# Performance work log

Measured on AMD Instinct MI355X. Metric: run time of the kernel, lower is better.

## Reference

```python
import jax, jax.numpy as jnp
import numpy as np

EPS_NORM = 1e-6
EPS_LN = 1e-5


def setup_inputs() -> dict:
    key = jax.random.key(0)
    ks = jax.random.split(key, 6)
    b, m, d = 8, 1024, 768
    n, p = 64, 16
    h = 2 * d
    x = jax.random.normal(ks[0], (b, m, d), dtype=jnp.float32)
    phi = jax.random.normal(ks[1], (n, p, d), dtype=jnp.float32)
    # per-expert LayerNorm affine params
    ln_g = jnp.ones((n, d), dtype=jnp.float32)
    ln_b = jnp.zeros((n, d), dtype=jnp.float32)
    # per-expert MLP weights (torch Linear default init ~ U(-1/sqrt(fan_in), ...); use scaled normal)
    w1 = jax.random.normal(ks[2], (n, d, h), dtype=jnp.float32) * (1.0 / np.sqrt(d))
    b1 = jax.random.normal(ks[3], (n, h), dtype=jnp.float32) * 0.01
    w2 = jax.random.normal(ks[4], (n, h, d), dtype=jnp.float32) * (1.0 / np.sqrt(h))
    b2 = jax.random.normal(ks[5], (n, d), dtype=jnp.float32) * 0.01
    return {"x": x, "phi": phi, "ln_g": ln_g, "ln_b": ln_b,
            "w1": w1, "b1": b1, "w2": w2, "b2": b2}


def _layernorm(x, g, b):
    mu = jnp.mean(x, axis=-1, keepdims=True)
    var = jnp.mean(jnp.square(x - mu), axis=-1, keepdims=True)
    return (x - mu) * jax.lax.rsqrt(var + EPS_LN) * g + b


def reference(x, phi, ln_g, ln_b, w1, b1, w2, b2):
    # normalize phi over axis=0 (expert axis), as in the torch __init__
    phi_n = phi * jax.lax.rsqrt(jnp.sum(jnp.square(phi), axis=0, keepdims=True) + EPS_NORM)
    bsz, m, d = x.shape
    n, p, _ = phi_n.shape
    # routing logits: [b, m, n, p]
    logits = jnp.einsum('bmd,npd->bmnp', x, phi_n)
    # dispatch: softmax over tokens m
    D = jax.nn.softmax(logits, axis=1)
    # combine: softmax over flattened slots (n*p)
    C = jax.nn.softmax(logits.reshape(bsz, m, n * p), axis=-1)
    # input slots: [b, n, p, d]
    Xs = jnp.einsum('bmd,bmnp->bnpd', x, D)
    # batched per-expert MLP: LN -> Linear -> GELU -> Linear
    hdn = _layernorm(Xs, ln_g[:, None, :], ln_b[:, None, :])
    hdn = jnp.einsum('bnpd,ndh->bnph', hdn, w1) + b1[:, None, :]
    hdn = jax.nn.gelu(hdn, approximate=False)
    Ys = jnp.einsum('bnph,nhd->bnpd', hdn, w2) + b2[:, None, :]
    # combine: [b, m, d]
    Ys = Ys.reshape(bsz, n * p, d)
    Y = jnp.einsum('bsd,bms->bmd', Ys, C)
    return Y
```

## Files before the change

kernel.cpp:

```cpp
#include <hip/hip_runtime.h>
#include <math.h>

#define B 8
#define M 1024
#define D 768
#define NEXP 64
#define P 16
#define H 1536
#define S 1024
#define EPS_NORM 1e-6f
#define EPS_LN   1e-5f

typedef unsigned short u16;
typedef __attribute__((ext_vector_type(8))) short bf16x8;
typedef __attribute__((ext_vector_type(4))) float f32x4;

__device__ __forceinline__ u16 f2bf(float f) {
    union { float f; unsigned u; } v; v.f = f;
    unsigned r = v.u + 0x7FFFu + ((v.u >> 16) & 1u);
    return (u16)(r >> 16);
}

__device__ __forceinline__ float gelu_exact(float x) {
    return 0.5f * x * (1.0f + erff(x * 0.70710678118654752440f));
}

#define GLL16(g, l) __builtin_amdgcn_global_load_lds( \
    (const __attribute__((address_space(1))) void*)(g), \
    (__attribute__((address_space(3))) void*)(l), 16, 0, 0)

__device__ __forceinline__ void mfma_core_128(const u16* __restrict__ Ag,
                                              const u16* __restrict__ Bg,
                                              int K, u16* As, u16* Bs,
                                              f32x4 (&acc)[4][4]) {
    const int t    = threadIdx.x;
    const int lane = t & 63;
    const int wave = t >> 6;
    const int wr   = (wave >> 1) << 6;
    const int wc   = (wave & 1) << 6;
    const int quad = lane >> 4;
    const int l16  = lane & 15;
    const u16* ga0 = Ag + (size_t)(t >> 2) * K + (t & 3) * 8;
    const u16* ga1 = ga0 + (size_t)64 * K;
    const u16* gb0 = Bg + (size_t)(t >> 2) * K + (t & 3) * 8;
    const u16* gb1 = gb0 + (size_t)64 * K;
    u16* la0 = As + t * 8;
    u16* la1 = la0 + 2048;
    u16* lb0 = Bs + t * 8;
    u16* lb1 = lb0 + 2048;
    const u16* arp = As + (wr + l16) * 32 + quad * 8;
    const u16* brp = Bs + (wc + l16) * 32 + quad * 8;
    for (int k0 = 0; k0 < K; k0 += 32) {
        __syncthreads();
        GLL16(ga0 + k0, la0);
        GLL16(ga1 + k0, la1);
        GLL16(gb0 + k0, lb0);
        GLL16(gb1 + k0, lb1);
        __syncthreads();
        bf16x8 af[4], bfr[4];
#pragma unroll
        for (int i = 0; i < 4; ++i) af[i]  = *(const bf16x8*)(arp + i * 512);
#pragma unroll
        for (int j = 0; j < 4; ++j) bfr[j] = *(const bf16x8*)(brp + j * 512);
#pragma unroll
        for (int i = 0; i < 4; ++i)
#pragma unroll
            for (int j = 0; j < 4; ++j)
                acc[i][j] = __builtin_amdgcn_mfma_f32_16x16x32_bf16(af[i], bfr[j], acc[i][j], 0, 0, 0);
    }
}

__device__ __forceinline__ void mfma_core_bf32(const u16* __restrict__ Ag, int K,
                                               const float* __restrict__ Bg, int ldb,
                                               u16* As, u16* Bs,
                                               f32x4 (&acc)[4][4]) {
    const int t    = threadIdx.x;
    const int lane = t & 63;
    const int wave = t >> 6;
    const int wr   = (wave >> 1) << 6;
    const int wc   = (wave & 1) << 6;
    const int quad = lane >> 4;
    const int l16  = lane & 15;
    const u16* ga0 = Ag + (size_t)(t >> 2) * K + (t & 3) * 8;
    const u16* ga1 = ga0 + (size_t)64 * K;
    u16* la0 = As + t * 8;
    u16* la1 = la0 + 2048;
    const int bcol = t & 127;
    const int kq   = (t >> 7) << 4;
    const float* bg0 = Bg + (size_t)kq * ldb + bcol;
    u16* lb = Bs + bcol * 40 + kq;
    const u16* arp = As + (wr + l16) * 32 + quad * 8;
    const u16* brp = Bs + (wc + l16) * 40 + quad * 8;
    for (int k0 = 0; k0 < K; k0 += 32) {
        const float* bg = bg0 + (size_t)k0 * ldb;
        __syncthreads();
        GLL16(ga0 + k0, la0);
        GLL16(ga1 + k0, la1);
        float f[16];
#pragma unroll
        for (int i = 0; i < 16; ++i) f[i] = bg[(size_t)i * ldb];
#pragma unroll
        for (int i = 0; i < 4; ++i) {
            ushort4 o;
            o.x = f2bf(f[i*4 + 0]); o.y = f2bf(f[i*4 + 1]);
            o.z = f2bf(f[i*4 + 2]); o.w = f2bf(f[i*4 + 3]);
            *(ushort4*)(lb + i * 4) = o;
        }
        __syncthreads();
        bf16x8 af[4], bfr[4];
#pragma unroll
        for (int i = 0; i < 4; ++i) af[i]  = *(const bf16x8*)(arp + i * 512);
#pragma unroll
        for (int j = 0; j < 4; ++j) bfr[j] = *(const bf16x8*)(brp + j * 640);
#pragma unroll
        for (int i = 0; i < 4; ++i)
#pragma unroll
            for (int j = 0; j < 4; ++j)
                acc[i][j] = __builtin_amdgcn_mfma_f32_16x16x32_bf16(af[i], bfr[j], acc[i][j], 0, 0, 0);
    }
}

#define EPI_VARS \
    const int t = threadIdx.x; const int lane = t & 63; const int wave = t >> 6; \
    const int wr = (wave >> 1) << 6; const int wc = (wave & 1) << 6; \
    const int quad = lane >> 4; const int l16 = lane & 15; (void)t;

#define ACC_INIT \
    f32x4 acc[4][4]; \
    _Pragma("unroll") for (int i = 0; i < 4; ++i) \
    _Pragma("unroll") for (int j = 0; j < 4; ++j) acc[i][j] = (f32x4){0.f, 0.f, 0.f, 0.f};

__global__ __launch_bounds__(256) void xprep_kernel(const float* __restrict__ x,
                                                    u16* __restrict__ xb,
                                                    u16* __restrict__ xT) {
    __shared__ float tile[64][65];
    int b = blockIdx.z;
    int m0 = blockIdx.y * 64, d0 = blockIdx.x * 64;
    int tt = threadIdx.x;
    int rr = tt >> 4, c4 = (tt & 15) * 4;
#pragma unroll
    for (int i = 0; i < 4; ++i) {
        int m = m0 + rr + i * 16;
        float4 v = *(const float4*)(x + ((size_t)b * M + m) * D + d0 + c4);
        tile[rr + i*16][c4 + 0] = v.x;
        tile[rr + i*16][c4 + 1] = v.y;
        tile[rr + i*16][c4 + 2] = v.z;
        tile[rr + i*16][c4 + 3] = v.w;
        ushort4 o;
        o.x = f2bf(v.x); o.y = f2bf(v.y); o.z = f2bf(v.z); o.w = f2bf(v.w);
        *(ushort4*)(xb + ((size_t)b * M + m) * D + d0 + c4) = o;
    }
    __syncthreads();
    int cr = tt >> 4, r4 = (tt & 15) * 4;
#pragma unroll
    for (int i = 0; i < 4; ++i) {
        int crow = cr + i * 16;
        ushort4 o;
        o.x = f2bf(tile[r4 + 0][crow]);
        o.y = f2bf(tile[r4 + 1][crow]);
        o.z = f2bf(tile[r4 + 2][crow]);
        o.w = f2bf(tile[r4 + 3][crow]);
        *(ushort4*)(xT + ((size_t)b * D + d0 + crow) * M + m0 + r4) = o;
    }
}

__global__ __launch_bounds__(256) void phi_norm_kernel(const float* __restrict__ phi,
                                                       u16* __restrict__ phinb) {
    int pos = blockIdx.x * 256 + threadIdx.x;
    float ss = 0.f;
#pragma unroll 4
    for (int nn = 0; nn < NEXP; ++nn) {
        float v = phi[nn * (P*D) + pos];
        ss += v * v;
    }
    float r = rsqrtf(ss + EPS_NORM);
#pragma unroll 4
    for (int nn = 0; nn < NEXP; ++nn)
        phinb[nn * (P*D) + pos] = f2bf(phi[nn * (P*D) + pos] * r);
}


__global__ __launch_bounds__(256) void gemm_logits_mfma(const u16* __restrict__ xb,
                                                        const u16* __restrict__ phinb,
                                                        float* __restrict__ logits) {
    __shared__ __align__(16) u16 As[4096], Bs[4096];
    ACC_INIT;
    const int row0 = blockIdx.y * 128, col0 = blockIdx.x * 128;
    mfma_core_128(xb + (size_t)row0 * D, phinb + (size_t)col0 * D, D, As, Bs, acc);
    EPI_VARS;
#pragma unroll
    for (int i = 0; i < 4; ++i)
#pragma unroll
        for (int j = 0; j < 4; ++j) {
            int col = col0 + wc + j*16 + l16;
#pragma unroll
            for (int r = 0; r < 4; ++r) {
                int row = row0 + wr + i*16 + quad*4 + r;
                logits[(size_t)row * S + col] = acc[i][j][r];
            }
        }
}

__global__ __launch_bounds__(256) void gemm_dispatch_mfma(const u16* __restrict__ DT,
                                                          const u16* __restrict__ xT,
                                                          float* __restrict__ Xs) {
    __shared__ __align__(16) u16 As[4096], Bs[4096];
    ACC_INIT;
    const int b = blockIdx.z;
    const int row0 = blockIdx.y * 128, col0 = blockIdx.x * 128;
    mfma_core_128(DT + ((size_t)b * S + row0) * M,
                  xT + ((size_t)b * D + col0) * M, M, As, Bs, acc);
    EPI_VARS;
#pragma unroll
    for (int i = 0; i < 4; ++i)
#pragma unroll
        for (int j = 0; j < 4; ++j) {
            int col = col0 + wc + j*16 + l16;
#pragma unroll
            for (int r = 0; r < 4; ++r) {
                int row = row0 + wr + i*16 + quad*4 + r;
                Xs[((size_t)b * S + row) * D + col] = acc[i][j][r];
            }
        }
}

__global__ __launch_bounds__(256) void gemm_mlp1_mfma(const u16* __restrict__ hdnE,
                                                      const float* __restrict__ w1,
                                                      const float* __restrict__ b1,
                                                      u16* __restrict__ h1) {
    __shared__ __align__(16) u16 As[4096], Bs[5120];
    ACC_INIT;
    const int n = blockIdx.z;
    const int col0 = blockIdx.x * 128;
    mfma_core_bf32(hdnE + (size_t)n * 128 * D, D,
                   w1 + (size_t)n * D * H + col0, H, As, Bs, acc);
    EPI_VARS;
#pragma unroll
    for (int i = 0; i < 4; ++i)
#pragma unroll
        for (int j = 0; j < 4; ++j) {
            int h = col0 + wc + j*16 + l16;
            float bias = b1[n * H + h];
#pragma unroll
            for (int r = 0; r < 4; ++r) {
                int row = wr + i*16 + quad*4 + r;
                h1[((size_t)n * 128 + row) * H + h] = f2bf(gelu_exact(acc[i][j][r] + bias));
            }
        }
}

__global__ __launch_bounds__(256) void gemm_mlp2_mfma(const u16* __restrict__ h1,
                                                      const float* __restrict__ w2,
                                                      const float* __restrict__ b2,
                                                      u16* __restrict__ YsT) {
    __shared__ __align__(16) u16 As[4096], Bs[5120];
    ACC_INIT;
    const int n = blockIdx.z;
    const int col0 = blockIdx.x * 128;
    mfma_core_bf32(h1 + (size_t)n * 128 * H, H,
                   w2 + (size_t)n * H * D + col0, D, As, Bs, acc);
    EPI_VARS;
#pragma unroll
    for (int i = 0; i < 4; ++i)
#pragma unroll
        for (int j = 0; j < 4; ++j) {
            int d = col0 + wc + j*16 + l16;
            float bias = b2[n * D + d];
            int bb = ((wr + i*16) >> 4);
            int p0 = quad * 4;
            ushort4 o;
            o.x = f2bf(acc[i][j][0] + bias);
            o.y = f2bf(acc[i][j][1] + bias);
            o.z = f2bf(acc[i][j][2] + bias);
            o.w = f2bf(acc[i][j][3] + bias);
            *(ushort4*)(YsT + ((size_t)bb * D + d) * S + n * P + p0) = o;
        }
}

__global__ __launch_bounds__(256) void gemm_combine_mfma(const u16* __restrict__ Cb,
                                                         const u16* __restrict__ YsT,
                                                         float* __restrict__ out) {
    __shared__ __align__(16) u16 As[4096], Bs[4096];
    ACC_INIT;
    const int b = blockIdx.z;
    const int row0 = blockIdx.y * 128, col0 = blockIdx.x * 128;
    mfma_core_128(Cb + ((size_t)b * M + row0) * S,
                  YsT + ((size_t)b * D + col0) * S, S, As, Bs, acc);
    EPI_VARS;
#pragma unroll
    for (int i = 0; i < 4; ++i)
#pragma unroll
        for (int j = 0; j < 4; ++j) {
            int col = col0 + wc + j*16 + l16;
#pragma unroll
            for (int r = 0; r < 4; ++r) {
                int row = row0 + wr + i*16 + quad*4 + r;
                out[((size_t)b * M + row) * D + col] = acc[i][j][r];
            }
        }
}


__global__ __launch_bounds__(256) void softmax_row_kernel(const float* __restrict__ in,
                                                          u16* __restrict__ outb) {
    __shared__ float red[4], red2[4];
    int row = blockIdx.x;
    int t = threadIdx.x;
    const float* rp = in + (size_t)row * S;
    float4 v = *(const float4*)(rp + t*4);
    float mx = fmaxf(fmaxf(v.x, v.y), fmaxf(v.z, v.w));
#pragma unroll
    for (int o = 1; o < 64; o <<= 1) mx = fmaxf(mx, __shfl_xor(mx, o));
    if ((t & 63) == 0) red[t >> 6] = mx;
    __syncthreads();
    mx = fmaxf(fmaxf(red[0], red[1]), fmaxf(red[2], red[3]));
    float4 e;
    e.x = expf(v.x - mx); e.y = expf(v.y - mx); e.z = expf(v.z - mx); e.w = expf(v.w - mx);
    float sum = e.x + e.y + e.z + e.w;
#pragma unroll
    for (int o = 1; o < 64; o <<= 1) sum += __shfl_xor(sum, o);
    if ((t & 63) == 0) red2[t >> 6] = sum;
    __syncthreads();
    sum = red2[0] + red2[1] + red2[2] + red2[3];
    float inv = 1.f / sum;
    ushort4 o4;
    o4.x = f2bf(e.x * inv); o4.y = f2bf(e.y * inv);
    o4.z = f2bf(e.z * inv); o4.w = f2bf(e.w * inv);
    *(ushort4*)(outb + (size_t)row * S + t*4) = o4;
}

__global__ __launch_bounds__(256) void colsm_partial_kernel(const float* __restrict__ logits,
                                                            float* __restrict__ pm,
                                                            float* __restrict__ pl) {
    int gid = blockIdx.x * 256 + threadIdx.x;
    int c   = gid >> 13;
    int col = gid & 8191;
    int b = col >> 10, s = col & (S - 1);
    const float* base = logits + ((size_t)b << 20) + ((size_t)(c * 128) << 10) + s;
    float mx = -INFINITY, l = 0.f;
    for (int m = 0; m < 128; ++m) {
        float v = base[(size_t)m << 10];
        float nm = fmaxf(mx, v);
        l = l * expf(mx - nm) + expf(v - nm);
        mx = nm;
    }
    pm[gid] = mx;
    pl[gid] = l;
}

__global__ __launch_bounds__(256) void colsm_combine_kernel(const float* __restrict__ pm,
                                                            const float* __restrict__ pl,
                                                            float* __restrict__ fm,
                                                            float* __restrict__ fl) {
    int col = blockIdx.x * 256 + threadIdx.x;
    float mx = -INFINITY;
#pragma unroll
    for (int c = 0; c < 8; ++c) mx = fmaxf(mx, pm[c * 8192 + col]);
    float l = 0.f;
#pragma unroll
    for (int c = 0; c < 8; ++c) l += pl[c * 8192 + col] * expf(pm[c * 8192 + col] - mx);
    fm[col] = mx;
    fl[col] = 1.f / l;
}

__global__ __launch_bounds__(256) void dt_transpose_kernel(const float* __restrict__ logits,
                                                           const float* __restrict__ fm,
                                                           const float* __restrict__ fl,
                                                           u16* __restrict__ DT) {
    __shared__ float tile[64][65];
    int b = blockIdx.z;
    int m0 = blockIdx.y * 64, s0 = blockIdx.x * 64;
    int tt = threadIdx.x;
    int rr = tt >> 4, c4 = (tt & 15) * 4;
    float4 fmv = *(const float4*)(fm + (size_t)b * S + s0 + c4);
    float4 flv = *(const float4*)(fl + (size_t)b * S + s0 + c4);
#pragma unroll
    for (int i = 0; i < 4; ++i) {
        float4 v = *(const float4*)(logits + ((size_t)b * M + m0 + rr + i*16) * S + s0 + c4);
        tile[rr + i*16][c4 + 0] = expf(v.x - fmv.x) * flv.x;
        tile[rr + i*16][c4 + 1] = expf(v.y - fmv.y) * flv.y;
        tile[rr + i*16][c4 + 2] = expf(v.z - fmv.z) * flv.z;
        tile[rr + i*16][c4 + 3] = expf(v.w - fmv.w) * flv.w;
    }
    __syncthreads();
    int cr = tt >> 4, r4 = (tt & 15) * 4;
#pragma unroll
    for (int i = 0; i < 4; ++i) {
        int crow = cr + i * 16;
        ushort4 o;
        o.x = f2bf(tile[r4 + 0][crow]);
        o.y = f2bf(tile[r4 + 1][crow]);
        o.z = f2bf(tile[r4 + 2][crow]);
        o.w = f2bf(tile[r4 + 3][crow]);
        *(ushort4*)(DT + ((size_t)b * S + s0 + crow) * M + m0 + r4) = o;
    }
}

__global__ __launch_bounds__(256) void layernorm_kernel(const float* __restrict__ Xs,
                                                        const float* __restrict__ g,
                                                        const float* __restrict__ bt,
                                                        u16* __restrict__ hdnE) {
    __shared__ float rs[4], rq[4];
    int row = blockIdx.x;
    int b = row >> 10;
    int n = (row >> 4) & (NEXP - 1);
    int p = row & 15;
    const float* rp = Xs + (size_t)row * D;
    u16* op = hdnE + ((size_t)n * 128 + b * 16 + p) * D;
    int t = threadIdx.x;
    float x0 = rp[t], x1 = rp[t + 256], x2 = rp[t + 512];
    float s  = x0 + x1 + x2;
    float sq = x0*x0 + x1*x1 + x2*x2;
#pragma unroll
    for (int o = 1; o < 64; o <<= 1) { s += __shfl_xor(s, o); sq += __shfl_xor(sq, o); }
    if ((t & 63) == 0) { rs[t >> 6] = s; rq[t >> 6] = sq; }
    __syncthreads();
    s  = rs[0] + rs[1] + rs[2] + rs[3];
    sq = rq[0] + rq[1] + rq[2] + rq[3];
    float mu  = s * (1.f / D);
    float var = sq * (1.f / D) - mu * mu;
    float inv = rsqrtf(var + EPS_LN);
    const float* gn = g  + n * D;
    const float* bn = bt + n * D;
    op[t]       = f2bf((x0 - mu) * inv * gn[t]       + bn[t]);
    op[t + 256] = f2bf((x1 - mu) * inv * gn[t + 256] + bn[t + 256]);
    op[t + 512] = f2bf((x2 - mu) * inv * gn[t + 512] + bn[t + 512]);
}

extern "C" void kernel_launch(void* const* d_in, const int* in_sizes, int n_in,
                              void* d_out, int out_size, void* d_ws, size_t ws_size,
                              hipStream_t stream) {
    const float* x    = (const float*)d_in[0];
    const float* phi  = (const float*)d_in[1];
    const float* ln_g = (const float*)d_in[2];
    const float* ln_b = (const float*)d_in[3];
    const float* w1   = (const float*)d_in[4];
    const float* b1   = (const float*)d_in[5];
    const float* w2   = (const float*)d_in[6];
    const float* b2   = (const float*)d_in[7];
    float* out = (float*)d_out;

    char* ws = (char*)d_ws;
    float* logits = (float*)(ws + 0);
    u16*   Cb     = (u16*)(ws + 33554432);
    u16*   xb     = (u16*)(ws + 50331648);
    u16*   DT     = (u16*)(ws + 62914560);
    u16*   xTb    = (u16*)(ws + 79691776);
    u16*   phinb  = (u16*)(ws + 92274688);
    u16*   hdnE   = (u16*)(ws + 93847552);
    float* pm     = (float*)(ws + 106430464);
    float* pl     = (float*)(ws + 106692608);
    float* fm     = (float*)(ws + 106954752);
    float* fl     = (float*)(ws + 106987520);
    float* Xs     = logits;
    u16*   h1     = xb;
    u16*   YsT    = xTb;

    xprep_kernel<<<dim3(12, 16, B), 256, 0, stream>>>(x, xb, xTb);
    phi_norm_kernel<<<48, 256, 0, stream>>>(phi, phinb);

    gemm_logits_mfma<<<dim3(8, 64), 256, 0, stream>>>(xb, phinb, logits);
    softmax_row_kernel<<<B * M, 256, 0, stream>>>(logits, Cb);
    colsm_partial_kernel<<<256, 256, 0, stream>>>(logits, pm, pl);
    colsm_combine_kernel<<<32, 256, 0, stream>>>(pm, pl, fm, fl);
    dt_transpose_kernel<<<dim3(16, 16, B), 256, 0, stream>>>(logits, fm, fl, DT);

    gemm_dispatch_mfma<<<dim3(6, 8, B), 256, 0, stream>>>(DT, xTb, Xs);
    layernorm_kernel<<<B * S, 256, 0, stream>>>(Xs, ln_g, ln_b, hdnE);

    gemm_mlp1_mfma<<<dim3(12, 1, NEXP), 256, 0, stream>>>(hdnE, w1, b1, h1);
    gemm_mlp2_mfma<<<dim3(6, 1, NEXP), 256, 0, stream>>>(h1, w2, b2, YsT);

    gemm_combine_mfma<<<dim3(6, 8, B), 256, 0, stream>>>(Cb, YsT, out);
}
```

Baseline: 795.9 us.

## Double-buffer LDS in MFMA GEMM cores and split column softmax into more chunks

Both GEMM core loops now use two LDS buffers: the next K-slice is prefetched (async global-to-LDS for bf16 operands, register loads plus bf16 conversion for fp32 weights) while MFMAs run on the current slice, and one barrier per iteration is removed. LDS allocations in all GEMM kernels double. Separately, the column-softmax partial pass splits the 1024 tokens into 32 chunks of 32 instead of 8 chunks of 128, launching four times as many threads to raise parallelism; the combine kernel reduces 32 partials and the workspace offsets move. Higher LDS use may lower occupancy, and holding prefetched floats in registers raises register pressure.

```diff
diff --git a/kernel.cpp b/kernel.cpp
--- a/kernel.cpp
+++ b/kernel.cpp
@@ -45,28 +45,36 @@
     const u16* gb0 = Bg + (size_t)(t >> 2) * K + (t & 3) * 8;
     const u16* gb1 = gb0 + (size_t)64 * K;
     u16* la0 = As + t * 8;
-    u16* la1 = la0 + 2048;
     u16* lb0 = Bs + t * 8;
-    u16* lb1 = lb0 + 2048;
     const u16* arp = As + (wr + l16) * 32 + quad * 8;
     const u16* brp = Bs + (wc + l16) * 32 + quad * 8;
+    GLL16(ga0, la0);
+    GLL16(ga1, la0 + 2048);
+    GLL16(gb0, lb0);
+    GLL16(gb1, lb0 + 2048);
+    int cur = 0;
     for (int k0 = 0; k0 < K; k0 += 32) {
         __syncthreads();
-        GLL16(ga0 + k0, la0);
-        GLL16(ga1 + k0, la1);
-        GLL16(gb0 + k0, lb0);
-        GLL16(gb1 + k0, lb1);
-        __syncthreads();
+        const int nxt = cur ^ 1;
+        if (k0 + 32 < K) {
+            GLL16(ga0 + k0 + 32, la0 + nxt * 4096);
+            GLL16(ga1 + k0 + 32, la0 + nxt * 4096 + 2048);
+            GLL16(gb0 + k0 + 32, lb0 + nxt * 4096);
+            GLL16(gb1 + k0 + 32, lb0 + nxt * 4096 + 2048);
+        }
+        const u16* ar = arp + cur * 4096;
+        const u16* br = brp + cur * 4096;
         bf16x8 af[4], bfr[4];
 #pragma unroll
-        for (int i = 0; i < 4; ++i) af[i]  = *(const bf16x8*)(arp + i * 512);
-#pragma unroll
-        for (int j = 0; j < 4; ++j) bfr[j] = *(const bf16x8*)(brp + j * 512);
+        for (int i = 0; i < 4; ++i) af[i]  = *(const bf16x8*)(ar + i * 512);
+#pragma unroll
+        for (int j = 0; j < 4; ++j) bfr[j] = *(const bf16x8*)(br + j * 512);
 #pragma unroll
         for (int i = 0; i < 4; ++i)
 #pragma unroll
             for (int j = 0; j < 4; ++j)
                 acc[i][j] = __builtin_amdgcn_mfma_f32_16x16x32_bf16(af[i], bfr[j], acc[i][j], 0, 0, 0);
+        cur = nxt;
     }
 }
 
@@ -84,21 +92,18 @@
     const u16* ga0 = Ag + (size_t)(t >> 2) * K + (t & 3) * 8;
     const u16* ga1 = ga0 + (size_t)64 * K;
     u16* la0 = As + t * 8;
-    u16* la1 = la0 + 2048;
     const int bcol = t & 127;
     const int kq   = (t >> 7) << 4;
     const float* bg0 = Bg + (size_t)kq * ldb + bcol;
     u16* lb = Bs + bcol * 40 + kq;
     const u16* arp = As + (wr + l16) * 32 + quad * 8;
     const u16* brp = Bs + (wc + l16) * 40 + quad * 8;
-    for (int k0 = 0; k0 < K; k0 += 32) {
-        const float* bg = bg0 + (size_t)k0 * ldb;
-        __syncthreads();
-        GLL16(ga0 + k0, la0);
-        GLL16(ga1 + k0, la1);
+    GLL16(ga0, la0);
+    GLL16(ga1, la0 + 2048);
+    {
         float f[16];
 #pragma unroll
-        for (int i = 0; i < 16; ++i) f[i] = bg[(size_t)i * ldb];
+        for (int i = 0; i < 16; ++i) f[i] = bg0[(size_t)i * ldb];
 #pragma unroll
         for (int i = 0; i < 4; ++i) {
             ushort4 o;
@@ -106,17 +111,43 @@
             o.z = f2bf(f[i*4 + 2]); o.w = f2bf(f[i*4 + 3]);
             *(ushort4*)(lb + i * 4) = o;
         }
+    }
+    int cur = 0;
+    for (int k0 = 0; k0 < K; k0 += 32) {
         __syncthreads();
+        const int nxt = cur ^ 1;
+        const bool pf = (k0 + 32 < K);
+        float f[16];
+        if (pf) {
+            GLL16(ga0 + k0 + 32, la0 + nxt * 4096);
+            GLL16(ga1 + k0 + 32, la0 + nxt * 4096 + 2048);
+            const float* bg = bg0 + (size_t)(k0 + 32) * ldb;
+#pragma unroll
+            for (int i = 0; i < 16; ++i) f[i] = bg[(size_t)i * ldb];
+        }
+        const u16* ar = arp + cur * 4096;
+        const u16* br = brp + cur * 5120;
         bf16x8 af[4], bfr[4];
 #pragma unroll
-        for (int i = 0; i < 4; ++i) af[i]  = *(const bf16x8*)(arp + i * 512);
-#pragma unroll
-        for (int j = 0; j < 4; ++j) bfr[j] = *(const bf16x8*)(brp + j * 640);
+        for (int i = 0; i < 4; ++i) af[i]  = *(const bf16x8*)(ar + i * 512);
+#pragma unroll
+        for (int j = 0; j < 4; ++j) bfr[j] = *(const bf16x8*)(br + j * 640);
 #pragma unroll
         for (int i = 0; i < 4; ++i)
 #pragma unroll
             for (int j = 0; j < 4; ++j)
                 acc[i][j] = __builtin_amdgcn_mfma_f32_16x16x32_bf16(af[i], bfr[j], acc[i][j], 0, 0, 0);
+        if (pf) {
+            u16* lbn = lb + nxt * 5120;
+#pragma unroll
+            for (int i = 0; i < 4; ++i) {
+                ushort4 o;
+                o.x = f2bf(f[i*4 + 0]); o.y = f2bf(f[i*4 + 1]);
+                o.z = f2bf(f[i*4 + 2]); o.w = f2bf(f[i*4 + 3]);
+                *(ushort4*)(lbn + i * 4) = o;
+            }
+        }
+        cur = nxt;
     }
 }
 
@@ -183,7 +214,7 @@
 __global__ __launch_bounds__(256) void gemm_logits_mfma(const u16* __restrict__ xb,
                                                         const u16* __restrict__ phinb,
                                                         float* __restrict__ logits) {
-    __shared__ __align__(16) u16 As[4096], Bs[4096];
+    __shared__ __align__(16) u16 As[8192], Bs[8192];
     ACC_INIT;
     const int row0 = blockIdx.y * 128, col0 = blockIdx.x * 128;
     mfma_core_128(xb + (size_t)row0 * D, phinb + (size_t)col0 * D, D, As, Bs, acc);
@@ -204,7 +235,7 @@
 __global__ __launch_bounds__(256) void gemm_dispatch_mfma(const u16* __restrict__ DT,
                                                           const u16* __restrict__ xT,
                                                           float* __restrict__ Xs) {
-    __shared__ __align__(16) u16 As[4096], Bs[4096];
+    __shared__ __align__(16) u16 As[8192], Bs[8192];
     ACC_INIT;
     const int b = blockIdx.z;
     const int row0 = blockIdx.y * 128, col0 = blockIdx.x * 128;
@@ -228,7 +259,7 @@
                                                       const float* __restrict__ w1,
                                                       const float* __restrict__ b1,
                                                       u16* __restrict__ h1) {
-    __shared__ __align__(16) u16 As[4096], Bs[5120];
+    __shared__ __align__(16) u16 As[8192], Bs[10240];
     ACC_INIT;
     const int n = blockIdx.z;
     const int col0 = blockIdx.x * 128;
@@ -253,7 +284,7 @@
                                                       const float* __restrict__ w2,
                                                       const float* __restrict__ b2,
                                                       u16* __restrict__ YsT) {
-    __shared__ __align__(16) u16 As[4096], Bs[5120];
+    __shared__ __align__(16) u16 As[8192], Bs[10240];
     ACC_INIT;
     const int n = blockIdx.z;
     const int col0 = blockIdx.x * 128;
@@ -280,7 +311,7 @@
 __global__ __launch_bounds__(256) void gemm_combine_mfma(const u16* __restrict__ Cb,
                                                          const u16* __restrict__ YsT,
                                                          float* __restrict__ out) {
-    __shared__ __align__(16) u16 As[4096], Bs[4096];
+    __shared__ __align__(16) u16 As[8192], Bs[8192];
     ACC_INIT;
     const int b = blockIdx.z;
     const int row0 = blockIdx.y * 128, col0 = blockIdx.x * 128;
@@ -336,9 +367,9 @@
     int c   = gid >> 13;
     int col = gid & 8191;
     int b = col >> 10, s = col & (S - 1);
-    const float* base = logits + ((size_t)b << 20) + ((size_t)(c * 128) << 10) + s;
+    const float* base = logits + ((size_t)b << 20) + ((size_t)(c * 32) << 10) + s;
     float mx = -INFINITY, l = 0.f;
-    for (int m = 0; m < 128; ++m) {
+    for (int m = 0; m < 32; ++m) {
         float v = base[(size_t)m << 10];
         float nm = fmaxf(mx, v);
         l = l * expf(mx - nm) + expf(v - nm);
@@ -355,10 +386,10 @@
     int col = blockIdx.x * 256 + threadIdx.x;
     float mx = -INFINITY;
 #pragma unroll
-    for (int c = 0; c < 8; ++c) mx = fmaxf(mx, pm[c * 8192 + col]);
+    for (int c = 0; c < 32; ++c) mx = fmaxf(mx, pm[c * 8192 + col]);
     float l = 0.f;
 #pragma unroll
-    for (int c = 0; c < 8; ++c) l += pl[c * 8192 + col] * expf(pm[c * 8192 + col] - mx);
+    for (int c = 0; c < 32; ++c) l += pl[c * 8192 + col] * expf(pm[c * 8192 + col] - mx);
     fm[col] = mx;
     fl[col] = 1.f / l;
 }
@@ -449,9 +480,9 @@
     u16*   phinb  = (u16*)(ws + 92274688);
     u16*   hdnE   = (u16*)(ws + 93847552);
     float* pm     = (float*)(ws + 106430464);
-    float* pl     = (float*)(ws + 106692608);
-    float* fm     = (float*)(ws + 106954752);
-    float* fl     = (float*)(ws + 106987520);
+    float* pl     = (float*)(ws + 107479040);
+    float* fm     = (float*)(ws + 108527616);
+    float* fl     = (float*)(ws + 108560384);
     float* Xs     = logits;
     u16*   h1     = xb;
     u16*   YsT    = xTb;
@@ -461,7 +492,7 @@
 
     gemm_logits_mfma<<<dim3(8, 64), 256, 0, stream>>>(xb, phinb, logits);
     softmax_row_kernel<<<B * M, 256, 0, stream>>>(logits, Cb);
-    colsm_partial_kernel<<<256, 256, 0, stream>>>(logits, pm, pl);
+    colsm_partial_kernel<<<1024, 256, 0, stream>>>(logits, pm, pl);
     colsm_combine_kernel<<<32, 256, 0, stream>>>(pm, pl, fm, fl);
     dt_transpose_kernel<<<dim3(16, 16, B), 256, 0, stream>>>(logits, fm, fl, DT);
 
```

Measured after the change: 800.1 us. No clear change (+0.5%).
